# Kernel optimization log

Measured on AMD Instinct MI355X. Metric: run time of the kernel, lower is better.

The kernel has to match this reference:

```python
import jax, jax.numpy as jnp
import numpy as np

MARGIN = 0.3
IN_FEATURES = 128
NUM_CLASSES = 100
BATCH = 4096


def setup_inputs() -> dict:
    key = jax.random.key(0)
    k1, k2, k3, k4 = jax.random.split(key, 4)
    embeddings = jax.random.normal(k1, (BATCH, IN_FEATURES), dtype=jnp.float32)
    labels = jax.random.randint(k2, (BATCH,), 0, NUM_CLASSES, dtype=jnp.int64)
    # nn.Linear params (kaiming-uniform-ish scale)
    bound = 1.0 / np.sqrt(IN_FEATURES)
    fc_w = jax.random.uniform(k3, (NUM_CLASSES, IN_FEATURES), jnp.float32, -bound, bound)
    fc_b = jax.random.uniform(k4, (NUM_CLASSES,), jnp.float32, -bound, bound)
    return {"embeddings": embeddings, "labels": labels, "fc_w": fc_w, "fc_b": fc_b}


def _triplet_hard(emb, labels, margin):
    # pairwise squared euclidean distances: ||a||^2 + ||b||^2 - 2 a.b
    sq = jnp.sum(emb * emb, axis=1)  # [B]
    d2 = sq[:, None] + sq[None, :] - 2.0 * (emb @ emb.T)
    dist = jnp.sqrt(jnp.clip(d2, 1e-12))  # [B, B]
    same = labels[:, None] == labels[None, :]  # [B, B] (diag True, as in torch)
    neg_inf = jnp.float32(-jnp.inf)
    pos_inf = jnp.float32(jnp.inf)
    ap = jnp.max(jnp.where(same, dist, neg_inf), axis=1)  # hardest positive
    an = jnp.min(jnp.where(same, pos_inf, dist), axis=1)  # hardest negative
    # MarginRankingLoss(target=1): mean(relu(-(an - ap) + margin))
    return jnp.mean(jax.nn.relu(ap - an + margin))


def _cross_entropy(logits, labels):
    logp = jax.nn.log_softmax(logits, axis=-1)
    return -jnp.mean(jnp.take_along_axis(logp, labels[:, None], axis=1)[:, 0])


def reference(embeddings, labels, fc_w, fc_b):
    logits = embeddings @ fc_w.T + fc_b  # [B, C]
    triplet = _triplet_hard(embeddings, labels, MARGIN)
    ce = _cross_entropy(logits, labels)
    return triplet + ce
```

## Files before the change

kernel.cpp:

```cpp
#include <hip/hip_runtime.h>
#include <math.h>

#define BATCH 4096
#define DIM 128
#define NCLS 100
#define MARGIN 0.3f
#define NTILE 272
#define GRID_MAIN 528

typedef __attribute__((ext_vector_type(8))) short short8;
typedef __attribute__((ext_vector_type(4))) float f32x4;

__device__ __forceinline__ unsigned short f2bf(float f) {
    unsigned int u = __float_as_uint(f);
    unsigned int r = (u + 0x7FFFu + ((u >> 16) & 1u)) >> 16;
    return (unsigned short)r;
}
__device__ __forceinline__ float bf2f(unsigned short b) {
    return __uint_as_float(((unsigned int)b) << 16);
}

#define ENC_MAX_ID 0x80000000u
#define ENC_MIN_ID 0x403FFFFFu
__device__ __forceinline__ unsigned int enc_max(float v) {
    return (__float_as_uint(v) >> 1) | 0x80000000u;
}
__device__ __forceinline__ float dec_max(unsigned int k) {
    return __uint_as_float((k & 0x7FFFFFFFu) << 1);
}
__device__ __forceinline__ unsigned int enc_min(float v) {
    return 0x7FFFFFFFu - (__float_as_uint(v) >> 1);
}
__device__ __forceinline__ float dec_min(unsigned int k) {
    return __uint_as_float((0x7FFFFFFFu - k) << 1);
}


__global__ __launch_bounds__(256) void prep_kernel(
        const float* __restrict__ emb, const float* __restrict__ fcw,
        unsigned short* __restrict__ ebf, float* __restrict__ sq,
        unsigned short* __restrict__ wbf, unsigned int* __restrict__ fanz) {
    int bid = blockIdx.x, tid = threadIdx.x;
    if (bid < 256) {
        int wave = tid >> 6, lane = tid & 63;
        unsigned int* dstg = reinterpret_cast<unsigned int*>(ebf) + bid * 1024;
        #pragma unroll
        for (int r = 0; r < 4; ++r) {
            int rowl = wave * 4 + r;
            int row = bid * 16 + rowl;
            const float2* src = reinterpret_cast<const float2*>(emb + row * DIM);
            float2 xy = src[lane];
            unsigned short b0 = f2bf(xy.x), b1 = f2bf(xy.y);
            float y0 = bf2f(b0), y1 = bf2f(b1);
            dstg[(lane >> 2) * 64 + rowl * 4 + (lane & 3)] =
                ((unsigned int)b1 << 16) | (unsigned int)b0;
            float acc = y0 * y0 + y1 * y1;
            #pragma unroll
            for (int off = 1; off < 64; off <<= 1) acc += __shfl_xor(acc, off, 64);
            if (lane == 0) sq[row] = acc;
        }
    } else {
        int idx = (bid - 256) * 256 + tid;
        for (int k = idx; k < 112 * DIM; k += 512) {
            int cls = k >> 7, d = k & 127;
            int dst = (cls >> 4) * 2048 + (d >> 3) * 128 + (cls & 15) * 8 + (d & 7);
            wbf[dst] = (k < NCLS * DIM) ? f2bf(fcw[k]) : (unsigned short)0;
        }
        for (int w = idx; w < 8194; w += 512)
            fanz[w] = 0;
    }
}

__global__ __launch_bounds__(256) void main_kernel(
        const unsigned short* __restrict__ ebf, const unsigned short* __restrict__ wbf,
        const float* __restrict__ sq, const int* __restrict__ labels,
        const float* __restrict__ fcb,
        unsigned int* __restrict__ maxk, unsigned int* __restrict__ mink,
        float* __restrict__ ce_sum, int* __restrict__ ticket,
        float* __restrict__ out) {
    __shared__ float lg[16][128];
    __shared__ unsigned int colk[512];
    __shared__ unsigned short bstage[2][2048];
    __shared__ int lastFlag;
    int bid = blockIdx.x, tid = threadIdx.x;
    int wave = tid >> 6, lane = tid & 63;
    int lm = lane & 15, lq = lane >> 4;

    if (bid < NTILE) {
        int c = 0, rem = bid;
        while (rem >= 2 * c + 2) { rem -= 2 * c + 2; ++c; }
        int rowgrp = rem;
        int chunk  = c;

        int rbase = rowgrp * 128 + wave * 32;
        const unsigned short* apt = ebf + (rbase >> 4) * 2048 + lane * 8;
        short8 a0 = *reinterpret_cast<const short8*>(apt);
        short8 a1 = *reinterpret_cast<const short8*>(apt + 512);
        short8 a2 = *reinterpret_cast<const short8*>(apt + 1024);
        short8 a3 = *reinterpret_cast<const short8*>(apt + 1536);
        short8 a4 = *reinterpret_cast<const short8*>(apt + 2048);
        short8 a5 = *reinterpret_cast<const short8*>(apt + 2560);
        short8 a6 = *reinterpret_cast<const short8*>(apt + 3072);
        short8 a7 = *reinterpret_cast<const short8*>(apt + 3584);

        int labr[8];
        float sqr[8];
        #pragma unroll
        for (int g = 0; g < 2; ++g)
            #pragma unroll
            for (int r = 0; r < 4; ++r) {
                labr[g * 4 + r] = labels[rbase + g * 16 + lq * 4 + r];
                sqr[g * 4 + r]  = sq[rbase + g * 16 + lq * 4 + r];
            }

        colk[tid] = 0; colk[256 + tid] = 0;

        float rmax[8], rmin[8];
        #pragma unroll
        for (int r = 0; r < 8; ++r) { rmax[r] = -INFINITY; rmin[r] = INFINITY; }

        int cbase = chunk * 256;
        const unsigned short* btile = ebf + (cbase >> 4) * 2048 + wave * 512 + lane * 8;
        uint4 breg = *reinterpret_cast<const uint4*>(btile);

        for (int ct = 0; ct < 16; ++ct) {
            *reinterpret_cast<uint4*>(&bstage[ct & 1][wave * 512 + lane * 8]) = breg;
            if (ct < 15)
                breg = *reinterpret_cast<const uint4*>(btile + (ct + 1) * 2048);
            __syncthreads();

            const unsigned short* bb = &bstage[ct & 1][lane * 8];
            short8 b0 = *reinterpret_cast<const short8*>(bb);
            short8 b1 = *reinterpret_cast<const short8*>(bb + 512);
            short8 b2 = *reinterpret_cast<const short8*>(bb + 1024);
            short8 b3 = *reinterpret_cast<const short8*>(bb + 1536);
            f32x4 c0 = {0.f, 0.f, 0.f, 0.f};
            f32x4 c1 = {0.f, 0.f, 0.f, 0.f};
            c0 = __builtin_amdgcn_mfma_f32_16x16x32_bf16(a0, b0, c0, 0, 0, 0);
            c1 = __builtin_amdgcn_mfma_f32_16x16x32_bf16(a4, b0, c1, 0, 0, 0);
            c0 = __builtin_amdgcn_mfma_f32_16x16x32_bf16(a1, b1, c0, 0, 0, 0);
            c1 = __builtin_amdgcn_mfma_f32_16x16x32_bf16(a5, b1, c1, 0, 0, 0);
            c0 = __builtin_amdgcn_mfma_f32_16x16x32_bf16(a2, b2, c0, 0, 0, 0);
            c1 = __builtin_amdgcn_mfma_f32_16x16x32_bf16(a6, b2, c1, 0, 0, 0);
            c0 = __builtin_amdgcn_mfma_f32_16x16x32_bf16(a3, b3, c0, 0, 0, 0);
            c1 = __builtin_amdgcn_mfma_f32_16x16x32_bf16(a7, b3, c1, 0, 0, 0);

            int col = cbase + ct * 16 + lm;
            float sqc = sq[col];
            int lc = labels[col];
            float cmax = -INFINITY, cmin = INFINITY;
            #pragma unroll
            for (int r = 0; r < 4; ++r) {
                float v0 = fmaxf(fmaf(c0[r], -2.0f, sqc) + sqr[r], 0.f);
                bool s0 = (lc == labr[r]);
                rmax[r] = s0 ? fmaxf(rmax[r], v0) : rmax[r];
                rmin[r] = s0 ? rmin[r] : fminf(rmin[r], v0);
                cmax    = s0 ? fmaxf(cmax, v0) : cmax;
                cmin    = s0 ? cmin : fminf(cmin, v0);
                float v1 = fmaxf(fmaf(c1[r], -2.0f, sqc) + sqr[4 + r], 0.f);
                bool s1 = (lc == labr[4 + r]);
                rmax[4 + r] = s1 ? fmaxf(rmax[4 + r], v1) : rmax[4 + r];
                rmin[4 + r] = s1 ? rmin[4 + r] : fminf(rmin[4 + r], v1);
                cmax        = s1 ? fmaxf(cmax, v1) : cmax;
                cmin        = s1 ? cmin : fminf(cmin, v1);
            }
            cmax = fmaxf(cmax, __shfl_xor(cmax, 16, 64));
            cmax = fmaxf(cmax, __shfl_xor(cmax, 32, 64));
            cmin = fminf(cmin, __shfl_xor(cmin, 16, 64));
            cmin = fminf(cmin, __shfl_xor(cmin, 32, 64));
            if (lq == 0) {
                atomicMax(&colk[ct * 16 + lm], enc_max(fmaxf(cmax, 0.f)));
                atomicMax(&colk[256 + ct * 16 + lm], enc_min(fmaxf(cmin, 0.f)));
            }
        }
        #pragma unroll
        for (int off = 1; off < 16; off <<= 1) {
            #pragma unroll
            for (int r = 0; r < 8; ++r) {
                rmax[r] = fmaxf(rmax[r], __shfl_xor(rmax[r], off, 64));
                rmin[r] = fminf(rmin[r], __shfl_xor(rmin[r], off, 64));
            }
        }
        if (lm == 0) {
            #pragma unroll
            for (int g = 0; g < 2; ++g)
                #pragma unroll
                for (int r = 0; r < 4; ++r) {
                    int row = rbase + g * 16 + lq * 4 + r;
                    unsigned int kx = enc_max(fmaxf(rmax[g * 4 + r], 0.f));
                    unsigned int kn = enc_min(fmaxf(rmin[g * 4 + r], 0.f));
                    if (kx != ENC_MAX_ID)
                        __hip_atomic_fetch_max(&maxk[row], kx,
                                               __ATOMIC_RELAXED, __HIP_MEMORY_SCOPE_AGENT);
                    if (kn != ENC_MIN_ID)
                        __hip_atomic_fetch_max(&mink[row], kn,
                                               __ATOMIC_RELAXED, __HIP_MEMORY_SCOPE_AGENT);
                }
        }
        __syncthreads();
        {
            unsigned int kx = colk[tid], kn = colk[256 + tid];
            int col = cbase + tid;
            if (kx > ENC_MAX_ID)
                __hip_atomic_fetch_max(&maxk[col], kx,
                                       __ATOMIC_RELAXED, __HIP_MEMORY_SCOPE_AGENT);
            if (kn != 0 && kn != ENC_MIN_ID)
                __hip_atomic_fetch_max(&mink[col], kn,
                                       __ATOMIC_RELAXED, __HIP_MEMORY_SCOPE_AGENT);
        }
    } else {
        int R0 = (bid - NTILE) * 16;
        lg[tid >> 4][112 + (tid & 15)] = -INFINITY;

        const unsigned short* apt = ebf + (R0 >> 4) * 2048 + lane * 8;
        short8 a0 = *reinterpret_cast<const short8*>(apt);
        short8 a1 = *reinterpret_cast<const short8*>(apt + 512);
        short8 a2 = *reinterpret_cast<const short8*>(apt + 1024);
        short8 a3 = *reinterpret_cast<const short8*>(apt + 1536);

        for (int t = wave * 2; t < 7 && t < wave * 2 + 2; ++t) {
            int cls = t * 16 + lm;
            const unsigned short* bp = wbf + t * 2048 + lane * 8;
            short8 b0 = *reinterpret_cast<const short8*>(bp);
            short8 b1 = *reinterpret_cast<const short8*>(bp + 512);
            short8 b2 = *reinterpret_cast<const short8*>(bp + 1024);
            short8 b3 = *reinterpret_cast<const short8*>(bp + 1536);
            f32x4 c = {0.f, 0.f, 0.f, 0.f};
            c = __builtin_amdgcn_mfma_f32_16x16x32_bf16(a0, b0, c, 0, 0, 0);
            c = __builtin_amdgcn_mfma_f32_16x16x32_bf16(a1, b1, c, 0, 0, 0);
            c = __builtin_amdgcn_mfma_f32_16x16x32_bf16(a2, b2, c, 0, 0, 0);
            c = __builtin_amdgcn_mfma_f32_16x16x32_bf16(a3, b3, c, 0, 0, 0);
            float bias = (cls < NCLS) ? fcb[cls] : -INFINITY;
            #pragma unroll
            for (int r = 0; r < 4; ++r)
                lg[lq * 4 + r][t * 16 + lm] = c[r] + bias;
        }
        __syncthreads();
        float cacc = 0.f;
        #pragma unroll
        for (int i = 0; i < 4; ++i) {
            int r = wave * 4 + i;
            float x0 = lg[r][lane], x1 = lg[r][lane + 64];
            float m = fmaxf(x0, x1);
            #pragma unroll
            for (int off = 1; off < 64; off <<= 1) m = fmaxf(m, __shfl_xor(m, off, 64));
            float s = expf(x0 - m) + expf(x1 - m);
            #pragma unroll
            for (int off = 1; off < 64; off <<= 1) s += __shfl_xor(s, off, 64);
            if (lane == 0) {
                int lab = labels[R0 + r];
                cacc += (m + logf(s)) - lg[r][lab];
            }
        }
        __syncthreads();
        if (lane == 0) lg[0][wave] = cacc;
        __syncthreads();
        if (tid == 0) {
            float bsum = lg[0][0] + lg[0][1] + lg[0][2] + lg[0][3];
            __hip_atomic_fetch_add(ce_sum, bsum,
                                   __ATOMIC_RELAXED, __HIP_MEMORY_SCOPE_AGENT);
        }
    }

    __syncthreads();
    asm volatile("s_waitcnt vmcnt(0)" ::: "memory");
    if (tid == 0) {
        int old = __hip_atomic_fetch_add(ticket, 1,
                                         __ATOMIC_RELAXED, __HIP_MEMORY_SCOPE_AGENT);
        lastFlag = (old == GRID_MAIN - 1);
    }
    __syncthreads();
    if (lastFlag) {
        float acc = 0.f;
        #pragma unroll
        for (int rr = 0; rr < 16; ++rr) {
            int row = rr * 256 + tid;
            unsigned int kx = __hip_atomic_load(&maxk[row], __ATOMIC_RELAXED,
                                                __HIP_MEMORY_SCOPE_AGENT);
            unsigned int kn = __hip_atomic_load(&mink[row], __ATOMIC_RELAXED,
                                                __HIP_MEMORY_SCOPE_AGENT);
            float ap = sqrtf(fmaxf(dec_max(kx), 1e-12f));
            float an = sqrtf(fmaxf(dec_min(kn), 1e-12f));
            acc += fmaxf(ap - an + MARGIN, 0.f);
        }
        float* red = reinterpret_cast<float*>(lg);
        red[tid] = acc;
        __syncthreads();
        for (int s = 128; s > 0; s >>= 1) {
            if (tid < s) red[tid] += red[tid + s];
            __syncthreads();
        }
        if (tid == 0) {
            float ces = __hip_atomic_load(ce_sum, __ATOMIC_RELAXED,
                                          __HIP_MEMORY_SCOPE_AGENT);
            out[0] = (red[0] + ces) * (1.0f / BATCH);
        }
    }
}

extern "C" void kernel_launch(void* const* d_in, const int* in_sizes, int n_in,
                              void* d_out, int out_size, void* d_ws, size_t ws_size,
                              hipStream_t stream) {
    const float* emb    = (const float*)d_in[0];
    const int*   labels = (const int*)  d_in[1];
    const float* fcw    = (const float*)d_in[2];
    const float* fcb    = (const float*)d_in[3];
    float* out = (float*)d_out;

    char* ws = (char*)d_ws;
    unsigned short* ebf = (unsigned short*)(ws);
    unsigned short* wbf = (unsigned short*)(ws + 1048576);
    float* sq           = (float*)(ws + 1081344);
    char* fan           = ws + 1097728;
    int*   ticket       = (int*)(fan);
    float* ce_sum       = (float*)(fan + 4);
    unsigned int* maxk  = (unsigned int*)(fan + 8);
    unsigned int* mink  = (unsigned int*)(fan + 8 + 16384);

    prep_kernel<<<258, 256, 0, stream>>>(emb, fcw, ebf, sq, wbf,
                                         (unsigned int*)fan);
    main_kernel<<<GRID_MAIN, 256, 0, stream>>>(ebf, wbf, sq, labels, fcb,
                                               maxk, mink, ce_sum, ticket, out);
}
```

Measured before the change: 93.63 us.

## Fuse bf16 conversion and norm computation into main kernel, drop prep kernel

Removes the separate prep kernel that converted embeddings and fc weights to bf16 in a tiled layout and precomputed squared norms. The main kernel now loads fp32 rows directly, converts them in registers, and computes row and column squared norms on the fly, sharing column norms through shared memory. The fan-in buffers are zeroed with a hipMemsetAsync instead. This saves a kernel launch and a round trip through workspace memory, at the cost of redundant fp32 loads and conversions in every tile block, with no longer any coalesced tiled bf16 layout.

```diff
diff --git a/kernel.cpp b/kernel.cpp
--- a/kernel.cpp
+++ b/kernel.cpp
@@ -35,52 +35,43 @@
     return __uint_as_float((0x7FFFFFFFu - k) << 1);
 }
 
-
-__global__ __launch_bounds__(256) void prep_kernel(
-        const float* __restrict__ emb, const float* __restrict__ fcw,
-        unsigned short* __restrict__ ebf, float* __restrict__ sq,
-        unsigned short* __restrict__ wbf, unsigned int* __restrict__ fanz) {
-    int bid = blockIdx.x, tid = threadIdx.x;
-    if (bid < 256) {
-        int wave = tid >> 6, lane = tid & 63;
-        unsigned int* dstg = reinterpret_cast<unsigned int*>(ebf) + bid * 1024;
-        #pragma unroll
-        for (int r = 0; r < 4; ++r) {
-            int rowl = wave * 4 + r;
-            int row = bid * 16 + rowl;
-            const float2* src = reinterpret_cast<const float2*>(emb + row * DIM);
-            float2 xy = src[lane];
-            unsigned short b0 = f2bf(xy.x), b1 = f2bf(xy.y);
-            float y0 = bf2f(b0), y1 = bf2f(b1);
-            dstg[(lane >> 2) * 64 + rowl * 4 + (lane & 3)] =
-                ((unsigned int)b1 << 16) | (unsigned int)b0;
-            float acc = y0 * y0 + y1 * y1;
-            #pragma unroll
-            for (int off = 1; off < 64; off <<= 1) acc += __shfl_xor(acc, off, 64);
-            if (lane == 0) sq[row] = acc;
-        }
-    } else {
-        int idx = (bid - 256) * 256 + tid;
-        for (int k = idx; k < 112 * DIM; k += 512) {
-            int cls = k >> 7, d = k & 127;
-            int dst = (cls >> 4) * 2048 + (d >> 3) * 128 + (cls & 15) * 8 + (d & 7);
-            wbf[dst] = (k < NCLS * DIM) ? f2bf(fcw[k]) : (unsigned short)0;
-        }
-        for (int w = idx; w < 8194; w += 512)
-            fanz[w] = 0;
+__device__ __forceinline__ float4 ld4(const float* p) {
+    return *reinterpret_cast<const float4*>(p);
+}
+
+__device__ __forceinline__ short8 cvt8s(float4 f0, float4 f1, float* ss) {
+    float v[8] = {f0.x, f0.y, f0.z, f0.w, f1.x, f1.y, f1.z, f1.w};
+    short8 r;
+    float s = 0.f;
+    #pragma unroll
+    for (int i = 0; i < 8; ++i) {
+        unsigned short b = f2bf(v[i]);
+        float y = bf2f(b);
+        s += y * y;
+        r[i] = (short)b;
     }
-}
-
-__global__ __launch_bounds__(256) void main_kernel(
-        const unsigned short* __restrict__ ebf, const unsigned short* __restrict__ wbf,
-        const float* __restrict__ sq, const int* __restrict__ labels,
-        const float* __restrict__ fcb,
+    *ss = s;
+    return r;
+}
+__device__ __forceinline__ short8 cvt8n(float4 f0, float4 f1) {
+    float v[8] = {f0.x, f0.y, f0.z, f0.w, f1.x, f1.y, f1.z, f1.w};
+    short8 r;
+    #pragma unroll
+    for (int i = 0; i < 8; ++i) r[i] = (short)f2bf(v[i]);
+    return r;
+}
+
+
+__global__ __launch_bounds__(256) void fused_kernel(
+        const float* __restrict__ emb, const int* __restrict__ labels,
+        const float* __restrict__ fcw, const float* __restrict__ fcb,
         unsigned int* __restrict__ maxk, unsigned int* __restrict__ mink,
         float* __restrict__ ce_sum, int* __restrict__ ticket,
         float* __restrict__ out) {
     __shared__ float lg[16][128];
     __shared__ unsigned int colk[512];
     __shared__ unsigned short bstage[2][2048];
+    __shared__ float colsqw[16][4][16];
     __shared__ int lastFlag;
     int bid = blockIdx.x, tid = threadIdx.x;
     int wave = tid >> 6, lane = tid & 63;
@@ -93,25 +84,36 @@
         int chunk  = c;
 
         int rbase = rowgrp * 128 + wave * 32;
-        const unsigned short* apt = ebf + (rbase >> 4) * 2048 + lane * 8;
-        short8 a0 = *reinterpret_cast<const short8*>(apt);
-        short8 a1 = *reinterpret_cast<const short8*>(apt + 512);
-        short8 a2 = *reinterpret_cast<const short8*>(apt + 1024);
-        short8 a3 = *reinterpret_cast<const short8*>(apt + 1536);
-        short8 a4 = *reinterpret_cast<const short8*>(apt + 2048);
-        short8 a5 = *reinterpret_cast<const short8*>(apt + 2560);
-        short8 a6 = *reinterpret_cast<const short8*>(apt + 3072);
-        short8 a7 = *reinterpret_cast<const short8*>(apt + 3584);
-
+
+        short8 a[8];
+        float rsq[2] = {0.f, 0.f};
+        #pragma unroll
+        for (int g = 0; g < 2; ++g) {
+            #pragma unroll
+            for (int j = 0; j < 4; ++j) {
+                const float* p = emb + (rbase + g * 16 + lm) * DIM + j * 32 + lq * 8;
+                float ss;
+                a[g * 4 + j] = cvt8s(ld4(p), ld4(p + 4), &ss);
+                rsq[g] += ss;
+            }
+        }
+        #pragma unroll
+        for (int g = 0; g < 2; ++g) {
+            rsq[g] += __shfl_xor(rsq[g], 16, 64);
+            rsq[g] += __shfl_xor(rsq[g], 32, 64);
+        }
+        float sqr[8];
         int labr[8];
-        float sqr[8];
+        #pragma unroll
+        for (int r = 0; r < 4; ++r) {
+            sqr[r]     = __shfl(rsq[0], lq * 4 + r, 64);
+            sqr[4 + r] = __shfl(rsq[1], lq * 4 + r, 64);
+        }
         #pragma unroll
         for (int g = 0; g < 2; ++g)
             #pragma unroll
-            for (int r = 0; r < 4; ++r) {
+            for (int r = 0; r < 4; ++r)
                 labr[g * 4 + r] = labels[rbase + g * 16 + lq * 4 + r];
-                sqr[g * 4 + r]  = sq[rbase + g * 16 + lq * 4 + r];
-            }
 
         colk[tid] = 0; colk[256 + tid] = 0;
 
@@ -120,13 +122,22 @@
         for (int r = 0; r < 8; ++r) { rmax[r] = -INFINITY; rmin[r] = INFINITY; }
 
         int cbase = chunk * 256;
-        const unsigned short* btile = ebf + (cbase >> 4) * 2048 + wave * 512 + lane * 8;
-        uint4 breg = *reinterpret_cast<const uint4*>(btile);
+        const float* bp = emb + (cbase + (tid & 15)) * DIM + (tid >> 4) * 8;
+        float4 f0 = ld4(bp);
+        float4 f1 = ld4(bp + 4);
 
         for (int ct = 0; ct < 16; ++ct) {
-            *reinterpret_cast<uint4*>(&bstage[ct & 1][wave * 512 + lane * 8]) = breg;
-            if (ct < 15)
-                breg = *reinterpret_cast<const uint4*>(btile + (ct + 1) * 2048);
+            float part;
+            short8 bv = cvt8s(f0, f1, &part);
+            *reinterpret_cast<short8*>(&bstage[ct & 1][tid * 8]) = bv;
+            part += __shfl_xor(part, 16, 64);
+            part += __shfl_xor(part, 32, 64);
+            if (lane < 16) colsqw[ct][wave][lane] = part;
+            if (ct < 15) {
+                const float* np = bp + (ct + 1) * 16 * DIM;
+                f0 = ld4(np);
+                f1 = ld4(np + 4);
+            }
             __syncthreads();
 
             const unsigned short* bb = &bstage[ct & 1][lane * 8];
@@ -136,17 +147,18 @@
             short8 b3 = *reinterpret_cast<const short8*>(bb + 1536);
             f32x4 c0 = {0.f, 0.f, 0.f, 0.f};
             f32x4 c1 = {0.f, 0.f, 0.f, 0.f};
-            c0 = __builtin_amdgcn_mfma_f32_16x16x32_bf16(a0, b0, c0, 0, 0, 0);
-            c1 = __builtin_amdgcn_mfma_f32_16x16x32_bf16(a4, b0, c1, 0, 0, 0);
-            c0 = __builtin_amdgcn_mfma_f32_16x16x32_bf16(a1, b1, c0, 0, 0, 0);
-            c1 = __builtin_amdgcn_mfma_f32_16x16x32_bf16(a5, b1, c1, 0, 0, 0);
-            c0 = __builtin_amdgcn_mfma_f32_16x16x32_bf16(a2, b2, c0, 0, 0, 0);
-            c1 = __builtin_amdgcn_mfma_f32_16x16x32_bf16(a6, b2, c1, 0, 0, 0);
-            c0 = __builtin_amdgcn_mfma_f32_16x16x32_bf16(a3, b3, c0, 0, 0, 0);
-            c1 = __builtin_amdgcn_mfma_f32_16x16x32_bf16(a7, b3, c1, 0, 0, 0);
+            c0 = __builtin_amdgcn_mfma_f32_16x16x32_bf16(a[0], b0, c0, 0, 0, 0);
+            c1 = __builtin_amdgcn_mfma_f32_16x16x32_bf16(a[4], b0, c1, 0, 0, 0);
+            c0 = __builtin_amdgcn_mfma_f32_16x16x32_bf16(a[1], b1, c0, 0, 0, 0);
+            c1 = __builtin_amdgcn_mfma_f32_16x16x32_bf16(a[5], b1, c1, 0, 0, 0);
+            c0 = __builtin_amdgcn_mfma_f32_16x16x32_bf16(a[2], b2, c0, 0, 0, 0);
+            c1 = __builtin_amdgcn_mfma_f32_16x16x32_bf16(a[6], b2, c1, 0, 0, 0);
+            c0 = __builtin_amdgcn_mfma_f32_16x16x32_bf16(a[3], b3, c0, 0, 0, 0);
+            c1 = __builtin_amdgcn_mfma_f32_16x16x32_bf16(a[7], b3, c1, 0, 0, 0);
 
             int col = cbase + ct * 16 + lm;
-            float sqc = sq[col];
+            float sqc = (colsqw[ct][0][lm] + colsqw[ct][1][lm]) +
+                        (colsqw[ct][2][lm] + colsqw[ct][3][lm]);
             int lc = labels[col];
             float cmax = -INFINITY, cmin = INFINITY;
             #pragma unroll
@@ -212,28 +224,34 @@
         int R0 = (bid - NTILE) * 16;
         lg[tid >> 4][112 + (tid & 15)] = -INFINITY;
 
-        const unsigned short* apt = ebf + (R0 >> 4) * 2048 + lane * 8;
-        short8 a0 = *reinterpret_cast<const short8*>(apt);
-        short8 a1 = *reinterpret_cast<const short8*>(apt + 512);
-        short8 a2 = *reinterpret_cast<const short8*>(apt + 1024);
-        short8 a3 = *reinterpret_cast<const short8*>(apt + 1536);
+        const float* apx = emb + (R0 + lm) * DIM + lq * 8;
+        short8 a0 = cvt8n(ld4(apx),      ld4(apx + 4));
+        short8 a1 = cvt8n(ld4(apx + 32), ld4(apx + 36));
+        short8 a2 = cvt8n(ld4(apx + 64), ld4(apx + 68));
+        short8 a3 = cvt8n(ld4(apx + 96), ld4(apx + 100));
 
         for (int t = wave * 2; t < 7 && t < wave * 2 + 2; ++t) {
             int cls = t * 16 + lm;
-            const unsigned short* bp = wbf + t * 2048 + lane * 8;
-            short8 b0 = *reinterpret_cast<const short8*>(bp);
-            short8 b1 = *reinterpret_cast<const short8*>(bp + 512);
-            short8 b2 = *reinterpret_cast<const short8*>(bp + 1024);
-            short8 b3 = *reinterpret_cast<const short8*>(bp + 1536);
-            f32x4 c = {0.f, 0.f, 0.f, 0.f};
-            c = __builtin_amdgcn_mfma_f32_16x16x32_bf16(a0, b0, c, 0, 0, 0);
-            c = __builtin_amdgcn_mfma_f32_16x16x32_bf16(a1, b1, c, 0, 0, 0);
-            c = __builtin_amdgcn_mfma_f32_16x16x32_bf16(a2, b2, c, 0, 0, 0);
-            c = __builtin_amdgcn_mfma_f32_16x16x32_bf16(a3, b3, c, 0, 0, 0);
+            short8 b0, b1, b2, b3;
+            if (cls < NCLS) {
+                const float* wp = fcw + cls * DIM + lq * 8;
+                b0 = cvt8n(ld4(wp),      ld4(wp + 4));
+                b1 = cvt8n(ld4(wp + 32), ld4(wp + 36));
+                b2 = cvt8n(ld4(wp + 64), ld4(wp + 68));
+                b3 = cvt8n(ld4(wp + 96), ld4(wp + 100));
+            } else {
+                short8 z = {0, 0, 0, 0, 0, 0, 0, 0};
+                b0 = z; b1 = z; b2 = z; b3 = z;
+            }
+            f32x4 cacc4 = {0.f, 0.f, 0.f, 0.f};
+            cacc4 = __builtin_amdgcn_mfma_f32_16x16x32_bf16(a0, b0, cacc4, 0, 0, 0);
+            cacc4 = __builtin_amdgcn_mfma_f32_16x16x32_bf16(a1, b1, cacc4, 0, 0, 0);
+            cacc4 = __builtin_amdgcn_mfma_f32_16x16x32_bf16(a2, b2, cacc4, 0, 0, 0);
+            cacc4 = __builtin_amdgcn_mfma_f32_16x16x32_bf16(a3, b3, cacc4, 0, 0, 0);
             float bias = (cls < NCLS) ? fcb[cls] : -INFINITY;
             #pragma unroll
             for (int r = 0; r < 4; ++r)
-                lg[lq * 4 + r][t * 16 + lm] = c[r] + bias;
+                lg[lq * 4 + r][t * 16 + lm] = cacc4[r] + bias;
         }
         __syncthreads();
         float cacc = 0.f;
@@ -279,21 +297,19 @@
                                                 __HIP_MEMORY_SCOPE_AGENT);
             unsigned int kn = __hip_atomic_load(&mink[row], __ATOMIC_RELAXED,
                                                 __HIP_MEMORY_SCOPE_AGENT);
-            float ap = sqrtf(fmaxf(dec_max(kx), 1e-12f));
-            float an = sqrtf(fmaxf(dec_min(kn), 1e-12f));
-            acc += fmaxf(ap - an + MARGIN, 0.f);
-        }
-        float* red = reinterpret_cast<float*>(lg);
-        red[tid] = acc;
-        __syncthreads();
-        for (int s = 128; s > 0; s >>= 1) {
-            if (tid < s) red[tid] += red[tid + s];
-            __syncthreads();
-        }
+            float pf = sqrtf(fmaxf(dec_max(kx), 1e-12f));
+            float nf = sqrtf(fmaxf(dec_min(kn), 1e-12f));
+            acc += fmaxf(pf - nf + MARGIN, 0.f);
+        }
+        #pragma unroll
+        for (int off = 1; off < 64; off <<= 1) acc += __shfl_xor(acc, off, 64);
+        if (lane == 0) lg[0][wave] = acc;
+        __syncthreads();
         if (tid == 0) {
             float ces = __hip_atomic_load(ce_sum, __ATOMIC_RELAXED,
                                           __HIP_MEMORY_SCOPE_AGENT);
-            out[0] = (red[0] + ces) * (1.0f / BATCH);
+            out[0] = ((lg[0][0] + lg[0][1] + lg[0][2] + lg[0][3]) + ces)
+                     * (1.0f / BATCH);
         }
     }
 }
@@ -308,17 +324,12 @@
     float* out = (float*)d_out;
 
     char* ws = (char*)d_ws;
-    unsigned short* ebf = (unsigned short*)(ws);
-    unsigned short* wbf = (unsigned short*)(ws + 1048576);
-    float* sq           = (float*)(ws + 1081344);
-    char* fan           = ws + 1097728;
-    int*   ticket       = (int*)(fan);
-    float* ce_sum       = (float*)(fan + 4);
-    unsigned int* maxk  = (unsigned int*)(fan + 8);
-    unsigned int* mink  = (unsigned int*)(fan + 8 + 16384);
-
-    prep_kernel<<<258, 256, 0, stream>>>(emb, fcw, ebf, sq, wbf,
-                                         (unsigned int*)fan);
-    main_kernel<<<GRID_MAIN, 256, 0, stream>>>(ebf, wbf, sq, labels, fcb,
-                                               maxk, mink, ce_sum, ticket, out);
-}
+    int*   ticket       = (int*)(ws);
+    float* ce_sum       = (float*)(ws + 4);
+    unsigned int* maxk  = (unsigned int*)(ws + 8);
+    unsigned int* mink  = (unsigned int*)(ws + 8 + 16384);
+
+    hipMemsetAsync(ws, 0, 8 + 32768, stream);
+    fused_kernel<<<GRID_MAIN, 256, 0, stream>>>(emb, labels, fcw, fcb,
+                                                maxk, mink, ce_sum, ticket, out);
+}
```

Result: no change. 94.90 us (+1.4%).
